# Kernel tuning notes

Hardware: AMD Instinct MI355X
Metric: run time of the kernel (lower is better)

The kernel has to match this reference:

```python
import jax, jax.numpy as jnp
import numpy as np

NEG_SLOPE = 0.2  # PyG GATv2Conv default leaky_relu slope


def _gatv2(x, src, dst, eattr, Wl, bl, Wr, br, We, att, bias, N):
    """GATv2Conv (concat heads, eval mode -> no dropout).
    x: [N, Fin], src/dst: [E], eattr: [E, Fe], att: [H, C]."""
    H, C = att.shape
    xl = (x @ Wl.T + bl).reshape(N, H, C)   # lin_l -> source features
    xr = (x @ Wr.T + br).reshape(N, H, C)   # lin_r -> target features
    ea = (eattr @ We.T).reshape(-1, H, C)   # lin_edge (no bias)
    m = xl[src] + xr[dst] + ea              # [E, H, C]
    m = jnp.where(m >= 0, m, NEG_SLOPE * m)
    logits = jnp.einsum('ehc,hc->eh', m, att)  # [E, H]
    # segment softmax over incoming edges of each target node
    lmax = jax.ops.segment_max(logits, dst, num_segments=N)  # self-loops -> nonempty
    ex = jnp.exp(logits - lmax[dst])
    denom = jax.ops.segment_sum(ex, dst, num_segments=N)
    alpha = ex / denom[dst]                 # [E, H]
    out = jax.ops.segment_sum(alpha[:, :, None] * xl[src], dst, num_segments=N)
    return out.reshape(N, H * C) + bias


def setup_inputs() -> dict:
    key = jax.random.key(0)
    ks = jax.random.split(key, 24)
    B, num_nodes, Fn, Fe, deg = 16, 5000, 64, 16, 32
    N = B * num_nodes
    E = N * deg
    s = 0.05
    inp = {
        'x': jax.random.normal(ks[0], (N, Fn), jnp.float32),
        'edge_index': jax.random.randint(ks[1], (2, E), 0, N, jnp.int64),
        'edge_attr': jax.random.normal(ks[2], (E, Fe), jnp.float32),
        'num_nodes': num_nodes,
        'W1l': jax.random.normal(ks[3], (9, Fn), jnp.float32) * s,
        'b1l': jnp.zeros((9,), jnp.float32),
        'W1r': jax.random.normal(ks[4], (9, Fn), jnp.float32) * s,
        'b1r': jnp.zeros((9,), jnp.float32),
        'We1': jax.random.normal(ks[5], (9, Fe), jnp.float32) * s,
        'att1': jax.random.normal(ks[6], (3, 3), jnp.float32) * s,
        'bias1': jnp.zeros((9,), jnp.float32),
        'W2l': jax.random.normal(ks[7], (20, 9), jnp.float32) * s,
        'b2l': jnp.zeros((20,), jnp.float32),
        'W2r': jax.random.normal(ks[8], (20, 9), jnp.float32) * s,
        'b2r': jnp.zeros((20,), jnp.float32),
        'We2': jax.random.normal(ks[9], (20, Fe), jnp.float32) * s,
        'att2': jax.random.normal(ks[10], (4, 5), jnp.float32) * s,
        'bias2': jnp.zeros((20,), jnp.float32),
        'fcW1': jax.random.normal(ks[11], (100, 20 * num_nodes), jnp.float32) * 0.01,
        'fcb1': jnp.zeros((100,), jnp.float32),
        'fcW2': jax.random.normal(ks[12], (10, 100), jnp.float32) * s,
        'fcb2': jnp.zeros((10,), jnp.float32),
        'fcW3': jax.random.normal(ks[13], (1, 10), jnp.float32) * s,
        'fcb3': jnp.zeros((1,), jnp.float32),
    }
    return inp


def reference(x, edge_index, edge_attr, num_nodes,
              W1l, b1l, W1r, b1r, We1, att1, bias1,
              W2l, b2l, W2r, b2r, We2, att2, bias2,
              fcW1, fcb1, fcW2, fcb2, fcW3, fcb3):
    N = x.shape[0]
    src0, dst0 = edge_index[0], edge_index[1]
    # add_self_loops=True, fill_value='mean': loop attr = mean of incoming edge attrs
    cnt = jax.ops.segment_sum(jnp.ones((src0.shape[0],), x.dtype), dst0, num_segments=N)
    loop_attr = jax.ops.segment_sum(edge_attr, dst0, num_segments=N) / jnp.maximum(cnt, 1.0)[:, None]
    nodes = jnp.arange(N)
    src = jnp.concatenate([src0, nodes])
    dst = jnp.concatenate([dst0, nodes])
    ea = jnp.concatenate([edge_attr, loop_attr], axis=0)

    h = _gatv2(x, src, dst, ea, W1l, b1l, W1r, b1r, We1, att1, bias1, N)
    h = jax.nn.relu(h)
    h = _gatv2(h, src, dst, ea, W2l, b2l, W2r, b2r, We2, att2, bias2, N)
    h = jax.nn.relu(h)

    B = N // num_nodes
    h = h.reshape(B, num_nodes * 20)
    h = jax.nn.relu(h @ fcW1.T + fcb1)
    h = jax.nn.relu(h @ fcW2.T + fcb2)
    return h @ fcW3.T + fcb3
```

## Files before the change

### kernel.cpp

```cpp
#include <hip/hip_runtime.h>
#include <math.h>

#define TPB   256
#define NPB   256
#define MAXNB 512
#define BCAP  10240
#define ITEMS 16
#define CPAD  16

static inline int gridFor(size_t n) { return (int)((n + TPB - 1) / TPB); }


__global__ void __launch_bounds__(TPB) k_lin1(
    const float* __restrict__ x,
    const float* __restrict__ Wl, const float* __restrict__ bl,
    const float* __restrict__ Wr, const float* __restrict__ br,
    float* __restrict__ xl, float* __restrict__ xr, int N)
{
  int idx = blockIdx.x * TPB + threadIdx.x;
  if (idx >= N * 18) return;
  int i = idx / 18, t = idx % 18;
  bool left = t < 9;
  int j = left ? t : t - 9;
  const float* W = (left ? Wl : Wr) + j * 64;
  float s = (left ? bl : br)[j];
  const float* xi = x + (size_t)i * 64;
#pragma unroll
  for (int f = 0; f < 64; f++) s = fmaf(xi[f], W[f], s);
  (left ? xl : xr)[(size_t)i * 9 + j] = s;
}

__global__ void __launch_bounds__(TPB) k_lin2(
    const float* __restrict__ h1, const float* __restrict__ bias1,
    const float* __restrict__ Wl, const float* __restrict__ bl,
    const float* __restrict__ Wr, const float* __restrict__ br,
    float* __restrict__ xl, float* __restrict__ xr, int N)
{
  int idx = blockIdx.x * TPB + threadIdx.x;
  if (idx >= N * 40) return;
  int i = idx / 40, t = idx % 40;
  float hr[9];
#pragma unroll
  for (int k = 0; k < 9; k++) hr[k] = fmaxf(h1[(size_t)i * 9 + k] + bias1[k], 0.0f);
  bool left = t < 20;
  int j = left ? t : t - 20;
  const float* W = (left ? Wl : Wr) + j * 9;
  float s = (left ? bl : br)[j];
#pragma unroll
  for (int k = 0; k < 9; k++) s = fmaf(hr[k], W[k], s);
  (left ? xl : xr)[(size_t)i * 20 + j] = s;
}


__global__ void __launch_bounds__(TPB) k_bin(
    const int* __restrict__ ei, int* __restrict__ bucketCntP,
    int2* __restrict__ staging, int E, int NB)
{
  __shared__ int hist[MAXNB];
  __shared__ int base[MAXNB];
  int tid = threadIdx.x;
  size_t tile0 = (size_t)blockIdx.x * (TPB * ITEMS);
  for (int i = tid; i < NB; i += TPB) hist[i] = 0;
  __syncthreads();
  for (int it = 0; it < ITEMS; ++it) {
    size_t e = tile0 + (size_t)it * TPB + tid;
    if (e < (size_t)E) {
      int dst = ei[(size_t)E + e];
      atomicAdd(&hist[dst >> 8], 1);
    }
  }
  __syncthreads();
  for (int i = tid; i < NB; i += TPB) {
    int c = hist[i];
    base[i] = c ? atomicAdd(&bucketCntP[(size_t)i * CPAD], c) : 0;
    hist[i] = 0;
  }
  __syncthreads();
  for (int it = 0; it < ITEMS; ++it) {
    size_t e = tile0 + (size_t)it * TPB + tid;
    if (e < (size_t)E) {
      int src = ei[e];
      int dst = ei[(size_t)E + e];
      int b = dst >> 8;
      int r = atomicAdd(&hist[b], 1);
      staging[(size_t)b * BCAP + base[b] + r] =
          make_int2((int)e | ((dst & 255) << 22), src);
    }
  }
}


__global__ void __launch_bounds__(MAXNB) k_scanb(
    const int* __restrict__ bucketCntP, int* __restrict__ bucketBase, int NB)
{
  __shared__ int s[MAXNB];
  int tid = threadIdx.x;
  int v = (tid < NB) ? bucketCntP[(size_t)tid * CPAD] : 0;
  s[tid] = v;
  __syncthreads();
  for (int off = 1; off < MAXNB; off <<= 1) {
    int u = (tid >= off) ? s[tid - off] : 0;
    __syncthreads();
    s[tid] += u;
    __syncthreads();
  }
  if (tid < NB) bucketBase[tid] = s[tid] - v;
}


__global__ void __launch_bounds__(TPB) k_csr(
    const int2* __restrict__ staging, const int* __restrict__ bucketCntP,
    const int* __restrict__ bucketBase,
    int* __restrict__ rowptr, int* __restrict__ degO,
    int* __restrict__ src_csr, int* __restrict__ eid_csr, int N)
{
  int b = blockIdx.x, tid = threadIdx.x;
  int n0 = b << 8;
  int recCnt = bucketCntP[(size_t)b * CPAD];
  int ebase = bucketBase[b];
  const int2* rec = staging + (size_t)b * BCAP;
  __shared__ int deg_s[NPB];
  __shared__ int pfx[NPB];
  __shared__ int cur[NPB];
  deg_s[tid] = 0;
  __syncthreads();
  for (int r = tid; r < recCnt; r += TPB)
    atomicAdd(&deg_s[(rec[r].x >> 22) & 255], 1);
  __syncthreads();
  pfx[tid] = deg_s[tid];
  __syncthreads();
  for (int off = 1; off < NPB; off <<= 1) {
    int u = (tid >= off) ? pfx[tid - off] : 0;
    __syncthreads();
    pfx[tid] += u;
    __syncthreads();
  }
  int excl = pfx[tid] - deg_s[tid];
  int n = n0 + tid;
  if (n < N) { rowptr[n] = ebase + excl; degO[n] = deg_s[tid]; }
  cur[tid] = ebase + excl;
  __syncthreads();
  for (int r = tid; r < recCnt; r += TPB) {
    int2 rc = rec[r];
    int dl = (rc.x >> 22) & 255;
    int eid = rc.x & 0x3FFFFF;
    int pos = atomicAdd(&cur[dl], 1);
    src_csr[pos] = rc.y;
    eid_csr[pos] = eid;
  }
}


__global__ void __launch_bounds__(TPB) k_reorder(
    const int* __restrict__ eid_csr, const float4* __restrict__ eattr4,
    float4* __restrict__ eac, int E)
{
  int idx = blockIdx.x * TPB + threadIdx.x;
  int slot = idx >> 2;
  int part = idx & 3;
  if (slot >= E) return;
  int eid = eid_csr[slot];
  eac[(size_t)slot * 4 + part] = eattr4[(size_t)eid * 4 + part];
}


template <int H, int C, int L, bool SEQ>
__global__ void __launch_bounds__(TPB) k_attn(
    const int* __restrict__ rowptr, const int* __restrict__ deg,
    const int* __restrict__ src_csr, const int* __restrict__ eid_csr,
    const float* __restrict__ ea_src,
    const float* __restrict__ xl, const float* __restrict__ xr,
    const float* __restrict__ We, const float* __restrict__ att,
    const float* __restrict__ bias,
    float* __restrict__ out, int N)
{
  constexpr int HC = H * C;
  int idx = blockIdx.x * TPB + threadIdx.x;
  if (idx >= N * H * L) return;
  int l = idx & (L - 1);
  int g = idx / L;
  int n = g / H, h = g - n * H;

  float w[C][16];
#pragma unroll
  for (int c = 0; c < C; c++)
#pragma unroll
    for (int f = 0; f < 16; f++) w[c][f] = We[(h * C + c) * 16 + f];
  float attv[C], xrv[C];
#pragma unroll
  for (int c = 0; c < C; c++) {
    attv[c] = att[h * C + c];
    xrv[c] = xr[(size_t)n * HC + h * C + c];
  }

  int r0 = rowptr[n];
  int dg = deg[n];

  float mx = -3.0e38f, den = 0.0f;
  float acc[C], ea_sum[C];
#pragma unroll
  for (int c = 0; c < C; c++) { acc[c] = 0.0f; ea_sum[c] = 0.0f; }

  for (int p = l; p < dg; p += L) {
    int pos = r0 + p;
    size_t abase = SEQ ? (size_t)pos * 16 : (size_t)eid_csr[pos] * 16;
    float a[16];
    const float4* a4 = (const float4*)(ea_src + abase);
#pragma unroll
    for (int k = 0; k < 4; k++) {
      float4 v = a4[k];
      a[4 * k + 0] = v.x; a[4 * k + 1] = v.y; a[4 * k + 2] = v.z; a[4 * k + 3] = v.w;
    }
    int srcn = src_csr[pos];
    const float* xs = xl + (size_t)srcn * HC + h * C;
    float xv[C];
#pragma unroll
    for (int c = 0; c < C; c++) xv[c] = xs[c];
    float lg = 0.0f;
#pragma unroll
    for (int c = 0; c < C; c++) {
      float ea = 0.0f;
#pragma unroll
      for (int f = 0; f < 16; f++) ea = fmaf(a[f], w[c][f], ea);
      ea_sum[c] += ea;
      float m = xv[c] + xrv[c] + ea;
      m = (m >= 0.0f) ? m : 0.2f * m;
      lg = fmaf(m, attv[c], lg);
    }
    float nm = fmaxf(mx, lg);
    float s = expf(mx - nm);
    float wE = expf(lg - nm);
    den = den * s + wE;
#pragma unroll
    for (int c = 0; c < C; c++) acc[c] = fmaf(acc[c], s, wE * xv[c]);
    mx = nm;
  }

#pragma unroll
  for (int off = 1; off < L; off <<= 1) {
    float omx  = __shfl_xor(mx, off, 64);
    float oden = __shfl_xor(den, off, 64);
    float nm = fmaxf(mx, omx);
    float s1 = expf(mx - nm);
    float s2 = expf(omx - nm);
    den = den * s1 + oden * s2;
#pragma unroll
    for (int c = 0; c < C; c++) {
      float oa = __shfl_xor(acc[c], off, 64);
      float oe = __shfl_xor(ea_sum[c], off, 64);
      acc[c] = acc[c] * s1 + oa * s2;
      ea_sum[c] += oe;
    }
    mx = nm;
  }

  {
    float invd = 1.0f / fmaxf((float)dg, 1.0f);
    const float* xs = xl + (size_t)n * HC + h * C;
    float xv[C];
#pragma unroll
    for (int c = 0; c < C; c++) xv[c] = xs[c];
    float lg = 0.0f;
#pragma unroll
    for (int c = 0; c < C; c++) {
      float m = xv[c] + xrv[c] + ea_sum[c] * invd;
      m = (m >= 0.0f) ? m : 0.2f * m;
      lg = fmaf(m, attv[c], lg);
    }
    float nm = fmaxf(mx, lg);
    float s = expf(mx - nm);
    float wE = expf(lg - nm);
    den = den * s + wE;
#pragma unroll
    for (int c = 0; c < C; c++) acc[c] = fmaf(acc[c], s, wE * xv[c]);
  }

  float inv = 1.0f / den;
  float* od = out + (size_t)n * HC + h * C;
  for (int c = l; c < C; c += L) {
    float v = acc[c] * inv;
    if (bias) v = fmaxf(v + bias[h * C + c], 0.0f);
    od[c] = v;
  }
}


__global__ void __launch_bounds__(TPB) k_fc1(
    const float* __restrict__ h2, const float* __restrict__ W,
    float* __restrict__ h3, int NN, int Kc)
{
  int o = blockIdx.x;
  int ks = blockIdx.y;
  int k0 = ks * Kc;
  int k1 = min(NN, k0 + Kc);
  float acc[16];
#pragma unroll
  for (int b = 0; b < 16; b++) acc[b] = 0.0f;
  const float* wo = W + (size_t)o * NN;
  for (int k = k0 + threadIdx.x; k < k1; k += TPB) {
    float w = wo[k];
#pragma unroll
    for (int b = 0; b < 16; b++) acc[b] = fmaf(h2[(size_t)b * NN + k], w, acc[b]);
  }
#pragma unroll
  for (int b = 0; b < 16; b++) {
    float v = acc[b];
#pragma unroll
    for (int off = 32; off > 0; off >>= 1) v += __shfl_down(v, off, 64);
    if ((threadIdx.x & 63) == 0) atomicAdd(&h3[b * 100 + o], v);
  }
}

__global__ void __launch_bounds__(TPB) k_fc23(
    const float* __restrict__ h3, const float* __restrict__ fcb1,
    const float* __restrict__ W2, const float* __restrict__ b2,
    const float* __restrict__ W3, const float* __restrict__ b3,
    float* __restrict__ out, int B)
{
  __shared__ float s3[32 * 100];
  __shared__ float s4[32 * 10];
  int tid = threadIdx.x;
  for (int t = tid; t < B * 100; t += TPB)
    s3[t] = fmaxf(h3[t] + fcb1[t % 100], 0.0f);
  __syncthreads();
  if (tid < B * 10) {
    int b = tid / 10, o = tid % 10;
    float s = b2[o];
#pragma unroll
    for (int k = 0; k < 100; k++) s = fmaf(s3[b * 100 + k], W2[o * 100 + k], s);
    s4[tid] = fmaxf(s, 0.0f);
  }
  __syncthreads();
  if (tid < B) {
    float s = b3[0];
#pragma unroll
    for (int k = 0; k < 10; k++) s = fmaf(s4[tid * 10 + k], W3[k], s);
    out[tid] = s;
  }
}


extern "C" void kernel_launch(void* const* d_in, const int* in_sizes, int n_in,
                              void* d_out, int out_size, void* d_ws, size_t ws_size,
                              hipStream_t stream) {
  const float* x      = (const float*)d_in[0];
  const int*   ei     = (const int*)d_in[1];
  const float* eattr  = (const float*)d_in[2];
  const float* W1l = (const float*)d_in[4];  const float* b1l = (const float*)d_in[5];
  const float* W1r = (const float*)d_in[6];  const float* b1r = (const float*)d_in[7];
  const float* We1 = (const float*)d_in[8];  const float* att1 = (const float*)d_in[9];
  const float* bias1 = (const float*)d_in[10];
  const float* W2l = (const float*)d_in[11]; const float* b2l = (const float*)d_in[12];
  const float* W2r = (const float*)d_in[13]; const float* b2r = (const float*)d_in[14];
  const float* We2 = (const float*)d_in[15]; const float* att2 = (const float*)d_in[16];
  const float* bias2 = (const float*)d_in[17];
  const float* fcW1 = (const float*)d_in[18]; const float* fcb1 = (const float*)d_in[19];
  const float* fcW2 = (const float*)d_in[20]; const float* fcb2 = (const float*)d_in[21];
  const float* fcW3 = (const float*)d_in[22]; const float* fcb3 = (const float*)d_in[23];
  float* out = (float*)d_out;

  const int N = in_sizes[0] / 64;
  const int E = in_sizes[2] / 16;
  const int num_nodes = in_sizes[18] / (100 * 20);
  const int B = N / num_nodes;
  const int NB = (N + NPB - 1) / NPB;

  char* base = (char*)d_ws;
  size_t off = 0;
  auto alloc = [&](size_t bytes) {
    size_t o = off; off += (bytes + 63) & ~(size_t)63; return o;
  };
  size_t o_bcnt   = alloc((size_t)NB * CPAD * 4);
  size_t o_h3     = alloc((size_t)B * 100 * 4);
  size_t zeroBytes = off;
  size_t o_bbase  = alloc((size_t)NB * 4);
  size_t o_stage  = alloc((size_t)NB * BCAP * 8);
  size_t o_rowptr = alloc((size_t)N * 4);
  size_t o_deg    = alloc((size_t)N * 4);
  size_t o_srcc   = alloc((size_t)E * 4);
  size_t o_eidc   = alloc((size_t)E * 4);
  size_t o_xl1    = alloc((size_t)N * 9 * 4);
  size_t o_xr1    = alloc((size_t)N * 9 * 4);
  size_t o_xl2    = alloc((size_t)N * 20 * 4);
  size_t o_xr2    = alloc((size_t)N * 20 * 4);
  size_t o_h1     = alloc((size_t)N * 9 * 4);
  size_t o_h2     = alloc((size_t)N * 20 * 4);
  size_t o_eac    = alloc((size_t)E * 16 * 4);
  bool seq = (off <= ws_size);

  int*   bcnt   = (int*)(base + o_bcnt);
  float* h3     = (float*)(base + o_h3);
  int*   bbase  = (int*)(base + o_bbase);
  int2*  stage  = (int2*)(base + o_stage);
  int*   rowptr = (int*)(base + o_rowptr);
  int*   deg    = (int*)(base + o_deg);
  int*   srcc   = (int*)(base + o_srcc);
  int*   eidc   = (int*)(base + o_eidc);
  float* xl1    = (float*)(base + o_xl1);
  float* xr1    = (float*)(base + o_xr1);
  float* xl2    = (float*)(base + o_xl2);
  float* xr2    = (float*)(base + o_xr2);
  float* h1     = (float*)(base + o_h1);
  float* h2     = (float*)(base + o_h2);
  float* eac    = (float*)(base + o_eac);

  hipMemsetAsync(d_ws, 0, zeroBytes, stream);

  k_lin1<<<gridFor((size_t)N * 18), TPB, 0, stream>>>(x, W1l, b1l, W1r, b1r, xl1, xr1, N);

  int binBlocks = (int)(((size_t)E + TPB * ITEMS - 1) / (TPB * ITEMS));
  k_bin<<<binBlocks, TPB, 0, stream>>>(ei, bcnt, stage, E, NB);
  k_scanb<<<1, MAXNB, 0, stream>>>(bcnt, bbase, NB);
  k_csr<<<NB, TPB, 0, stream>>>(stage, bcnt, bbase, rowptr, deg, srcc, eidc, N);
  if (seq)
    k_reorder<<<gridFor((size_t)E * 4), TPB, 0, stream>>>(
        eidc, (const float4*)eattr, (float4*)eac, E);

  if (seq)
    k_attn<3, 3, 8, true><<<gridFor((size_t)N * 3 * 8), TPB, 0, stream>>>(
        rowptr, deg, srcc, eidc, eac, xl1, xr1, We1, att1, nullptr, h1, N);
  else
    k_attn<3, 3, 8, false><<<gridFor((size_t)N * 3 * 8), TPB, 0, stream>>>(
        rowptr, deg, srcc, eidc, eattr, xl1, xr1, We1, att1, nullptr, h1, N);

  k_lin2<<<gridFor((size_t)N * 40), TPB, 0, stream>>>(h1, bias1, W2l, b2l, W2r, b2r, xl2, xr2, N);

  if (seq)
    k_attn<4, 5, 8, true><<<gridFor((size_t)N * 4 * 8), TPB, 0, stream>>>(
        rowptr, deg, srcc, eidc, eac, xl2, xr2, We2, att2, bias2, h2, N);
  else
    k_attn<4, 5, 8, false><<<gridFor((size_t)N * 4 * 8), TPB, 0, stream>>>(
        rowptr, deg, srcc, eidc, eattr, xl2, xr2, We2, att2, bias2, h2, N);

  const int NN = num_nodes * 20;
  const int KS = 16;
  const int Kc = (NN + KS - 1) / KS;
  dim3 g1(100, KS);
  k_fc1<<<g1, TPB, 0, stream>>>(h2, fcW1, h3, NN, Kc);
  k_fc23<<<1, TPB, 0, stream>>>(h3, fcb1, fcW2, fcb2, fcW3, fcb3, out, B);
  (void)out_size; (void)n_in;
}
```

Before: 800.3 us.

## Precompute per-edge projected edge features for both GAT layers in one pass

Replaces the edge-attribute reorder kernel with a projection kernel that gathers each edge's 16 attributes once in CSR order and multiplies by both We1 and We2, storing 9- and 20-wide projected features. The attention kernels then read the precomputed projections instead of redoing the 16-wide dot products per head, and they no longer load the weight matrix into registers. This cuts redundant FLOPs and register pressure, but total edge bytes grow from 16 to 29 floats per edge, and the workspace needed for the fast path grows too. If the workspace is too small, the fallback path is used.

```diff
diff --git a/kernel.cpp b/kernel.cpp
--- a/kernel.cpp
+++ b/kernel.cpp
@@ -151,24 +151,71 @@
 }
 
 
-__global__ void __launch_bounds__(TPB) k_reorder(
+__global__ void __launch_bounds__(TPB) k_eproj(
     const int* __restrict__ eid_csr, const float4* __restrict__ eattr4,
-    float4* __restrict__ eac, int E)
-{
-  int idx = blockIdx.x * TPB + threadIdx.x;
-  int slot = idx >> 2;
-  int part = idx & 3;
-  if (slot >= E) return;
-  int eid = eid_csr[slot];
-  eac[(size_t)slot * 4 + part] = eattr4[(size_t)eid * 4 + part];
-}
-
-
-template <int H, int C, int L, bool SEQ>
+    const float* __restrict__ We1, const float* __restrict__ We2,
+    float* __restrict__ p1, float* __restrict__ p2, int E)
+{
+  int tid = blockIdx.x * TPB + threadIdx.x;
+  int lane = tid & 15;
+  int g0 = tid >> 4;
+  int gstride = (gridDim.x * TPB) >> 4;
+
+  float w1[16], w2a[16], w2b[16];
+  {
+    int r1 = lane < 9 ? lane : 8;
+    const float4* q = (const float4*)(We1 + r1 * 16);
+    float4 v0 = q[0], v1 = q[1], v2 = q[2], v3 = q[3];
+    w1[0]=v0.x; w1[1]=v0.y; w1[2]=v0.z; w1[3]=v0.w;
+    w1[4]=v1.x; w1[5]=v1.y; w1[6]=v1.z; w1[7]=v1.w;
+    w1[8]=v2.x; w1[9]=v2.y; w1[10]=v2.z; w1[11]=v2.w;
+    w1[12]=v3.x; w1[13]=v3.y; w1[14]=v3.z; w1[15]=v3.w;
+  }
+  {
+    const float4* q = (const float4*)(We2 + lane * 16);
+    float4 v0 = q[0], v1 = q[1], v2 = q[2], v3 = q[3];
+    w2a[0]=v0.x; w2a[1]=v0.y; w2a[2]=v0.z; w2a[3]=v0.w;
+    w2a[4]=v1.x; w2a[5]=v1.y; w2a[6]=v1.z; w2a[7]=v1.w;
+    w2a[8]=v2.x; w2a[9]=v2.y; w2a[10]=v2.z; w2a[11]=v2.w;
+    w2a[12]=v3.x; w2a[13]=v3.y; w2a[14]=v3.z; w2a[15]=v3.w;
+  }
+  {
+    const float4* q = (const float4*)(We2 + (16 + (lane & 3)) * 16);
+    float4 v0 = q[0], v1 = q[1], v2 = q[2], v3 = q[3];
+    w2b[0]=v0.x; w2b[1]=v0.y; w2b[2]=v0.z; w2b[3]=v0.w;
+    w2b[4]=v1.x; w2b[5]=v1.y; w2b[6]=v1.z; w2b[7]=v1.w;
+    w2b[8]=v2.x; w2b[9]=v2.y; w2b[10]=v2.z; w2b[11]=v2.w;
+    w2b[12]=v3.x; w2b[13]=v3.y; w2b[14]=v3.z; w2b[15]=v3.w;
+  }
+
+  for (int s = g0; s < E; s += gstride) {
+    int eid = eid_csr[s];
+    const float4* a4 = eattr4 + (size_t)eid * 4;
+    float4 A0 = a4[0], A1 = a4[1], A2 = a4[2], A3 = a4[3];
+    float a[16];
+    a[0]=A0.x; a[1]=A0.y; a[2]=A0.z; a[3]=A0.w;
+    a[4]=A1.x; a[5]=A1.y; a[6]=A1.z; a[7]=A1.w;
+    a[8]=A2.x; a[9]=A2.y; a[10]=A2.z; a[11]=A2.w;
+    a[12]=A3.x; a[13]=A3.y; a[14]=A3.z; a[15]=A3.w;
+    float s1 = 0.0f, s2a = 0.0f, s2b = 0.0f;
+#pragma unroll
+    for (int f = 0; f < 16; f++) {
+      s1  = fmaf(a[f], w1[f],  s1);
+      s2a = fmaf(a[f], w2a[f], s2a);
+      s2b = fmaf(a[f], w2b[f], s2b);
+    }
+    if (lane < 9) p1[(size_t)s * 9 + lane] = s1;
+    p2[(size_t)s * 20 + lane] = s2a;
+    if (lane < 4) p2[(size_t)s * 20 + 16 + lane] = s2b;
+  }
+}
+
+
+template <int H, int C, int L, bool PROJ>
 __global__ void __launch_bounds__(TPB) k_attn(
     const int* __restrict__ rowptr, const int* __restrict__ deg,
     const int* __restrict__ src_csr, const int* __restrict__ eid_csr,
-    const float* __restrict__ ea_src,
+    const float* __restrict__ ea,
     const float* __restrict__ xl, const float* __restrict__ xr,
     const float* __restrict__ We, const float* __restrict__ att,
     const float* __restrict__ bias,
@@ -181,11 +228,13 @@
   int g = idx / L;
   int n = g / H, h = g - n * H;
 
-  float w[C][16];
-#pragma unroll
-  for (int c = 0; c < C; c++)
-#pragma unroll
-    for (int f = 0; f < 16; f++) w[c][f] = We[(h * C + c) * 16 + f];
+  float w[PROJ ? 1 : C][PROJ ? 1 : 16];
+  if constexpr (!PROJ) {
+#pragma unroll
+    for (int c = 0; c < C; c++)
+#pragma unroll
+      for (int f = 0; f < 16; f++) w[c][f] = We[(h * C + c) * 16 + f];
+  }
   float attv[C], xrv[C];
 #pragma unroll
   for (int c = 0; c < C; c++) {
@@ -203,13 +252,26 @@
 
   for (int p = l; p < dg; p += L) {
     int pos = r0 + p;
-    size_t abase = SEQ ? (size_t)pos * 16 : (size_t)eid_csr[pos] * 16;
-    float a[16];
-    const float4* a4 = (const float4*)(ea_src + abase);
-#pragma unroll
-    for (int k = 0; k < 4; k++) {
-      float4 v = a4[k];
-      a[4 * k + 0] = v.x; a[4 * k + 1] = v.y; a[4 * k + 2] = v.z; a[4 * k + 3] = v.w;
+    float eav[C];
+    if constexpr (PROJ) {
+      const float* pp = ea + (size_t)pos * HC + h * C;
+#pragma unroll
+      for (int c = 0; c < C; c++) eav[c] = pp[c];
+    } else {
+      float a[16];
+      const float4* a4 = (const float4*)(ea + (size_t)eid_csr[pos] * 16);
+#pragma unroll
+      for (int k = 0; k < 4; k++) {
+        float4 v = a4[k];
+        a[4 * k + 0] = v.x; a[4 * k + 1] = v.y; a[4 * k + 2] = v.z; a[4 * k + 3] = v.w;
+      }
+#pragma unroll
+      for (int c = 0; c < C; c++) {
+        float s = 0.0f;
+#pragma unroll
+        for (int f = 0; f < 16; f++) s = fmaf(a[f], w[c][f], s);
+        eav[c] = s;
+      }
     }
     int srcn = src_csr[pos];
     const float* xs = xl + (size_t)srcn * HC + h * C;
@@ -219,11 +281,8 @@
     float lg = 0.0f;
 #pragma unroll
     for (int c = 0; c < C; c++) {
-      float ea = 0.0f;
-#pragma unroll
-      for (int f = 0; f < 16; f++) ea = fmaf(a[f], w[c][f], ea);
-      ea_sum[c] += ea;
-      float m = xv[c] + xrv[c] + ea;
+      ea_sum[c] += eav[c];
+      float m = xv[c] + xrv[c] + eav[c];
       m = (m >= 0.0f) ? m : 0.2f * m;
       lg = fmaf(m, attv[c], lg);
     }
@@ -385,7 +444,8 @@
   size_t o_xr2    = alloc((size_t)N * 20 * 4);
   size_t o_h1     = alloc((size_t)N * 9 * 4);
   size_t o_h2     = alloc((size_t)N * 20 * 4);
-  size_t o_eac    = alloc((size_t)E * 16 * 4);
+  size_t o_p1     = alloc((size_t)E * 9 * 4);
+  size_t o_p2     = alloc((size_t)E * 20 * 4);
   bool seq = (off <= ws_size);
 
   int*   bcnt   = (int*)(base + o_bcnt);
@@ -402,7 +462,8 @@
   float* xr2    = (float*)(base + o_xr2);
   float* h1     = (float*)(base + o_h1);
   float* h2     = (float*)(base + o_h2);
-  float* eac    = (float*)(base + o_eac);
+  float* p1     = (float*)(base + o_p1);
+  float* p2     = (float*)(base + o_p2);
 
   hipMemsetAsync(d_ws, 0, zeroBytes, stream);
 
@@ -412,13 +473,13 @@
   k_bin<<<binBlocks, TPB, 0, stream>>>(ei, bcnt, stage, E, NB);
   k_scanb<<<1, MAXNB, 0, stream>>>(bcnt, bbase, NB);
   k_csr<<<NB, TPB, 0, stream>>>(stage, bcnt, bbase, rowptr, deg, srcc, eidc, N);
+
   if (seq)
-    k_reorder<<<gridFor((size_t)E * 4), TPB, 0, stream>>>(
-        eidc, (const float4*)eattr, (float4*)eac, E);
+    k_eproj<<<2048, TPB, 0, stream>>>(eidc, (const float4*)eattr, We1, We2, p1, p2, E);
 
   if (seq)
     k_attn<3, 3, 8, true><<<gridFor((size_t)N * 3 * 8), TPB, 0, stream>>>(
-        rowptr, deg, srcc, eidc, eac, xl1, xr1, We1, att1, nullptr, h1, N);
+        rowptr, deg, srcc, eidc, p1, xl1, xr1, nullptr, att1, nullptr, h1, N);
   else
     k_attn<3, 3, 8, false><<<gridFor((size_t)N * 3 * 8), TPB, 0, stream>>>(
         rowptr, deg, srcc, eidc, eattr, xl1, xr1, We1, att1, nullptr, h1, N);
@@ -427,7 +488,7 @@
 
   if (seq)
     k_attn<4, 5, 8, true><<<gridFor((size_t)N * 4 * 8), TPB, 0, stream>>>(
-        rowptr, deg, srcc, eidc, eac, xl2, xr2, We2, att2, bias2, h2, N);
+        rowptr, deg, srcc, eidc, p2, xl2, xr2, nullptr, att2, bias2, h2, N);
   else
     k_attn<4, 5, 8, false><<<gridFor((size_t)N * 4 * 8), TPB, 0, stream>>>(
         rowptr, deg, srcc, eidc, eattr, xl2, xr2, We2, att2, bias2, h2, N);
```

Measured after the change: 974.6 us. 21.8% more time.
